# Kernel optimization log

Hardware: AMD Instinct MI355X
Metric: run time of the kernel (lower is better)

The kernel has to match this reference:

```python
import jax, jax.numpy as jnp
import numpy as np

RES = 32  # voxel grid resolution per axis (cfg.MODEL.NEURAL_POINTS.VOXEL_RES)


def upsample_ac(x, s):
    """Bilinear upsample with align_corners=True. x: [B,C,h,w] -> [B,C,h*s,w*s]."""
    if s == 1:
        return x
    B, C, h, w = x.shape
    H, W = h * s, w * s
    ys = jnp.arange(H, dtype=x.dtype) * ((h - 1) / (H - 1))
    xs = jnp.arange(W, dtype=x.dtype) * ((w - 1) / (W - 1))
    y0 = jnp.floor(ys).astype(jnp.int32)
    x0 = jnp.floor(xs).astype(jnp.int32)
    y1 = jnp.minimum(y0 + 1, h - 1)
    x1 = jnp.minimum(x0 + 1, w - 1)
    wy = (ys - y0.astype(x.dtype))[:, None]  # [H,1]
    wx = (xs - x0.astype(x.dtype))[None, :]  # [1,W]
    top = x[:, :, y0, :]
    bot = x[:, :, y1, :]
    a = top[..., x0]; b = top[..., x1]; c = bot[..., x0]; d = bot[..., x1]
    return (a * (1 - wx) + b * wx) * (1 - wy) + (c * (1 - wx) + d * wx) * wy


def vox_closest(pos):
    """construct_vox_points_closest: per occupied voxel, index of point closest to
    the voxel's point centroid. pos: [N,3] -> [RES^3] int32 indices."""
    N = pos.shape[0]
    Vn = RES ** 3
    mn = pos.min(0)
    mx = pos.max(0)
    vsz = (mx - mn) / RES  # obtain_voxel_size_based_grid_res
    coord = jnp.clip(jnp.floor((pos - mn) / vsz).astype(jnp.int32), 0, RES - 1)
    vid = (coord[:, 0] * RES + coord[:, 1]) * RES + coord[:, 2]  # [N]
    cnt = jax.ops.segment_sum(jnp.ones((N,), pos.dtype), vid, Vn)
    cen = jax.ops.segment_sum(pos, vid, Vn) / jnp.maximum(cnt, 1.0)[:, None]
    d = jnp.sum((pos - cen[vid]) ** 2, axis=-1)  # [N] dist^2 to own-voxel centroid
    dmin = jax.ops.segment_min(d, vid, Vn)
    cand = jnp.where(d <= dmin[vid], jnp.arange(N, dtype=jnp.int32), N)
    midx = jax.ops.segment_min(cand, vid, Vn)
    return jnp.where(midx >= N, 0, midx)  # guard (rare) empty voxels


def reference(rgb, f1, f2, f3, points_pos, points_dir, W1, b1, W2, b2, points_mask):
    V, _, H, W = rgb.shape
    N = V * H * W
    C = 59
    # valid_index = where(points_mask == 1) (mask is all ones -> identity gather)
    valid = jnp.nonzero(points_mask[0] == 1, size=N, fill_value=0)[0]
    pos = points_pos[0, valid]          # [N,3]
    pdir = points_dir[0, valid]         # [N,3]
    # project_point_feats: upsample each pyramid level to full res, concat channels
    ups = [upsample_ac(rgb, 1), upsample_ac(f1, 2), upsample_ac(f2, 4), upsample_ac(f3, 8)]
    pif = jnp.concatenate(ups, axis=1)                       # [V,59,H,W]
    pif = jnp.transpose(pif, (0, 2, 3, 1)).reshape(N, C)     # [N,59]
    color = jax.lax.stop_gradient(jnp.transpose(rgb, (0, 2, 3, 1)).reshape(N, 3))
    pif = pif[valid]
    color = color[valid]
    emb = jnp.concatenate([pif, pdir], axis=-1)              # [N,62]
    midx = vox_closest(pos)                                  # [32768]
    sel_emb = emb[midx]
    sel_pos = pos[midx]
    sel_color = color[midx]
    sel_dir = pdir[midx]
    # point_mlp (premlp_init): 62 -> 256 -> 256
    h = jax.nn.relu(sel_emb @ W1 + b1)
    points_embedding = h @ W2 + b2
    return points_embedding, sel_pos, sel_color, sel_dir


def setup_inputs() -> dict:
    key = jax.random.key(0)
    ks = jax.random.split(key, 10)
    V, H, W = 8, 240, 320
    N = V * H * W
    return {
        "rgb": jax.random.uniform(ks[0], (V, 3, H, W), jnp.float32),
        "f1": jax.random.normal(ks[1], (V, 8, H // 2, W // 2), jnp.float32),
        "f2": jax.random.normal(ks[2], (V, 16, H // 4, W // 4), jnp.float32),
        "f3": jax.random.normal(ks[3], (V, 32, H // 8, W // 8), jnp.float32),
        "points_pos": jax.random.uniform(ks[4], (1, N, 3), jnp.float32),
        "points_dir": jax.random.normal(ks[5], (1, N, 3), jnp.float32),
        "W1": jax.random.normal(ks[6], (62, 256), jnp.float32) * 0.05,
        "b1": jnp.zeros((256,), jnp.float32),
        "W2": jax.random.normal(ks[7], (256, 256), jnp.float32) * 0.05,
        "b2": jnp.zeros((256,), jnp.float32),
        "points_mask": jnp.ones((1, N), jnp.int32),
    }
```

## Files before the change

kernel.cpp:

```cpp
#include <hip/hip_runtime.h>
#include <hip/hip_bf16.h>
#include <limits.h>
#include <stddef.h>

#define NPTS   614400
#define RESV   32
#define NVOX   (RESV*RESV*RESV)
#define IMG_H  240
#define IMG_W  320
#define IMG_HW (IMG_H*IMG_W)
#define INF    __builtin_inff()
#define CAP    64
#define CAPP   32
#define SPILLCAP 4096

typedef __attribute__((ext_vector_type(8))) short short8;
typedef __attribute__((ext_vector_type(4))) short s16x4;
typedef __attribute__((ext_vector_type(4))) float f32x4;
typedef float f32x4u __attribute__((ext_vector_type(4), aligned(4)));

__device__ __forceinline__ float fadd_(float a, float b){
#pragma clang fp contract(off)
  return a + b;
}
__device__ __forceinline__ float fsub_(float a, float b){
#pragma clang fp contract(off)
  return a - b;
}
__device__ __forceinline__ float fmul_(float a, float b){
#pragma clang fp contract(off)
  return a * b;
}
__device__ __forceinline__ float fdiv_(float a, float b){
#pragma clang fp contract(off)
  return a / b;
}

__device__ __forceinline__ short f2bf(float x){
  __hip_bfloat16 h = __float2bfloat16(x);
  return *reinterpret_cast<short*>(&h);
}

__global__ void k_prep(int* __restrict__ cnt, int* __restrict__ spillcnt,
                       const float* __restrict__ W1, const float* __restrict__ W2,
                       short* __restrict__ W1t, short* __restrict__ W2t,
                       const float* __restrict__ pos,
                       f32x4* __restrict__ pmin, f32x4* __restrict__ pmax,
                       const float* __restrict__ f1, const float* __restrict__ f2,
                       const float* __restrict__ f3,
                       float* __restrict__ f1t, float* __restrict__ f2t,
                       float* __restrict__ f3t, int tposed){
  int gid = blockIdx.x*blockDim.x + threadIdx.x;
  int stride = gridDim.x*blockDim.x;
  if (gid < NVOX) cnt[gid] = 0;
  if (gid == 0) *spillcnt = 0;
  if (gid < 256*64){
    int n = gid >> 6, k = gid & 63;
    W1t[gid] = (k < 62) ? f2bf(W1[k*256 + n]) : (short)0;
  } else if (gid < 256*64 + 256*256){
    int j = gid - 256*64;
    int n = j >> 8, k = j & 255;
    W2t[j] = f2bf(W2[k*256 + n]);
  }

  if (tposed){
    for (int p = gid; p < 8*19200; p += stride){
      int img = p / 19200, pix = p - img*19200;
      const float* s = f1 + (size_t)img*8*19200 + pix;
      float r[8];
      #pragma unroll
      for (int c = 0; c < 8; c++) r[c] = s[(size_t)c*19200];
      float* d = f1t + (size_t)p*8;
      *(f32x4*)&d[0] = (f32x4){r[0],r[1],r[2],r[3]};
      *(f32x4*)&d[4] = (f32x4){r[4],r[5],r[6],r[7]};
    }
    for (int p = gid; p < 8*4800; p += stride){
      int img = p / 4800, pix = p - img*4800;
      const float* s = f2 + (size_t)img*16*4800 + pix;
      float* d = f2t + (size_t)p*16;
      #pragma unroll
      for (int cq = 0; cq < 4; cq++){
        f32x4 v = { s[(size_t)(4*cq+0)*4800], s[(size_t)(4*cq+1)*4800],
                    s[(size_t)(4*cq+2)*4800], s[(size_t)(4*cq+3)*4800] };
        *(f32x4*)&d[4*cq] = v;
      }
    }
    for (int p = gid; p < 8*1200; p += stride){
      int img = p / 1200, pix = p - img*1200;
      const float* s = f3 + (size_t)img*32*1200 + pix;
      float* d = f3t + (size_t)p*32;
      #pragma unroll
      for (int cq = 0; cq < 8; cq++){
        f32x4 v = { s[(size_t)(4*cq+0)*1200], s[(size_t)(4*cq+1)*1200],
                    s[(size_t)(4*cq+2)*1200], s[(size_t)(4*cq+3)*1200] };
        *(f32x4*)&d[4*cq] = v;
      }
    }
  }

  const f32x4* p4 = (const f32x4*)pos;
  float mn[3] = {  INF,  INF,  INF };
  float mx[3] = { -INF, -INF, -INF };
  for (int t = gid; t < NPTS/4; t += stride){
    f32x4 a = p4[3*t+0], b = p4[3*t+1], c = p4[3*t+2];
    mn[0] = fminf(mn[0], fminf(fminf(a.x, a.w), fminf(b.z, c.y)));
    mx[0] = fmaxf(mx[0], fmaxf(fmaxf(a.x, a.w), fmaxf(b.z, c.y)));
    mn[1] = fminf(mn[1], fminf(fminf(a.y, b.x), fminf(b.w, c.z)));
    mx[1] = fmaxf(mx[1], fmaxf(fmaxf(a.y, b.x), fmaxf(b.w, c.z)));
    mn[2] = fminf(mn[2], fminf(fminf(a.z, b.y), fminf(c.x, c.w)));
    mx[2] = fmaxf(mx[2], fmaxf(fmaxf(a.z, b.y), fmaxf(c.x, c.w)));
  }
  #pragma unroll
  for (int off = 32; off >= 1; off >>= 1){
    #pragma unroll
    for (int c = 0; c < 3; c++){
      mn[c] = fminf(mn[c], __shfl_down(mn[c], off, 64));
      mx[c] = fmaxf(mx[c], __shfl_down(mx[c], off, 64));
    }
  }
  __shared__ float smn[4][3], smx[4][3];
  int lane = threadIdx.x & 63, w = threadIdx.x >> 6;
  if (lane == 0){
    #pragma unroll
    for (int c = 0; c < 3; c++){ smn[w][c] = mn[c]; smx[w][c] = mx[c]; }
  }
  __syncthreads();
  if (threadIdx.x == 0){
    f32x4 a, b;
    a.x = fminf(fminf(smn[0][0], smn[1][0]), fminf(smn[2][0], smn[3][0]));
    a.y = fminf(fminf(smn[0][1], smn[1][1]), fminf(smn[2][1], smn[3][1]));
    a.z = fminf(fminf(smn[0][2], smn[1][2]), fminf(smn[2][2], smn[3][2]));
    a.w = 0.f;
    b.x = fmaxf(fmaxf(smx[0][0], smx[1][0]), fmaxf(smx[2][0], smx[3][0]));
    b.y = fmaxf(fmaxf(smx[0][1], smx[1][1]), fmaxf(smx[2][1], smx[3][1]));
    b.z = fmaxf(fmaxf(smx[0][2], smx[1][2]), fmaxf(smx[2][2], smx[3][2]));
    b.w = 0.f;
    pmin[blockIdx.x] = a;
    pmax[blockIdx.x] = b;
  }
}

__device__ __forceinline__ void reduce_minmax(const f32x4* __restrict__ pmin,
                                              const f32x4* __restrict__ pmax,
                                              float mn[3], float vsz[3]){
  int t = threadIdx.x;
  f32x4 a = pmin[t], b = pmin[t+256];
  f32x4 c = pmax[t], d = pmax[t+256];
  float lmn[3] = { fminf(a.x,b.x), fminf(a.y,b.y), fminf(a.z,b.z) };
  float lmx[3] = { fmaxf(c.x,d.x), fmaxf(c.y,d.y), fmaxf(c.z,d.z) };
  #pragma unroll
  for (int off = 32; off >= 1; off >>= 1){
    #pragma unroll
    for (int k = 0; k < 3; k++){
      lmn[k] = fminf(lmn[k], __shfl_xor(lmn[k], off, 64));
      lmx[k] = fmaxf(lmx[k], __shfl_xor(lmx[k], off, 64));
    }
  }
  __shared__ float smn[4][3], smx[4][3];
  int lane = t & 63, w = t >> 6;
  if (lane == 0){
    #pragma unroll
    for (int k = 0; k < 3; k++){ smn[w][k] = lmn[k]; smx[w][k] = lmx[k]; }
  }
  __syncthreads();
  #pragma unroll
  for (int k = 0; k < 3; k++){
    mn[k] = fminf(fminf(smn[0][k], smn[1][k]), fminf(smn[2][k], smn[3][k]));
    float mx = fmaxf(fmaxf(smx[0][k], smx[1][k]), fmaxf(smx[2][k], smx[3][k]));
    vsz[k] = fdiv_(fsub_(mx, mn[k]), 32.0f);
  }
}

__global__ void k_scatter(const float* __restrict__ pos,
                          const f32x4* __restrict__ pmin, const f32x4* __restrict__ pmax,
                          int* __restrict__ cnt, int* __restrict__ slots,
                          int* __restrict__ spillcnt, int2* __restrict__ spill,
                          f32x4* __restrict__ slotpos, int haspp){
  float mn[3], vsz[3];
  reduce_minmax(pmin, pmax, mn, vsz);

  int i = blockIdx.x*blockDim.x + threadIdx.x;
  float P[3] = { pos[3*i+0], pos[3*i+1], pos[3*i+2] };
  int v = 0;
  #pragma unroll
  for (int k = 0; k < 3; k++){
    float tt = fdiv_(fsub_(P[k], mn[k]), vsz[k]);
    int cc = (int)floorf(tt);
    cc = min(max(cc, 0), RESV-1);
    v = v*RESV + cc;
  }
  int p = atomicAdd(&cnt[v], 1);
  if (haspp){
    if (p < CAPP){
      f32x4 e = { P[0], P[1], P[2], __int_as_float(i) };
      slotpos[(size_t)v*CAPP + p] = e;
    } else if (p < CAP){
      slots[v*CAP + p] = i;
    } else {
      int sp = atomicAdd(spillcnt, 1);
      if (sp < SPILLCAP){ int2 e; e.x = v; e.y = i; spill[sp] = e; }
    }
  } else {
    if (p < CAP){
      slots[v*CAP + p] = i;
    } else {
      int sp = atomicAdd(spillcnt, 1);
      if (sp < SPILLCAP){ int2 e; e.x = v; e.y = i; spill[sp] = e; }
    }
  }
}

__launch_bounds__(256)
__global__ void k_voxfull(const int* __restrict__ cnt, const int* __restrict__ slots,
                          const int* __restrict__ spillcnt, const int2* __restrict__ spill,
                          const f32x4* __restrict__ slotpos, int haspp,
                          const float* __restrict__ pos,
                          const float* __restrict__ pdir, const float* __restrict__ rgb,
                          const float* __restrict__ f1, const float* __restrict__ f2,
                          const float* __restrict__ f3,
                          const float* __restrict__ f1t, const float* __restrict__ f2t,
                          const float* __restrict__ f3t, int tposed,
                          float* __restrict__ selpos, float* __restrict__ selcol,
                          float* __restrict__ seldir, short* __restrict__ emb){
  __shared__ __align__(16) int skey[4][64];
  __shared__ f32x4 sposl[4][64];
  int lane = threadIdx.x & 63;
  int wv   = threadIdx.x >> 6;
  int v = blockIdx.x*4 + wv;

  f32x4 q = {0.f, 0.f, 0.f, 0.f};
  if (haspp) q = slotpos[(size_t)v*CAPP + (lane & (CAPP-1))];
  int n = cnt[v];

  int m = 0;
  unsigned long long ball = 0;
  float px = 0.f, py = 0.f, pz = 0.f;

  if (n > CAP){
    if (lane == 0){
      int sc = min(*spillcnt, SPILLCAP);
      float sx = 0.f, sy = 0.f, sz = 0.f; int last = -1;
      for (int i = 0; i < n; i++){
        int best = INT_MAX;
        for (int j = 0; j < CAP; j++){
          int id = (haspp && j < CAPP) ? __float_as_int(slotpos[(size_t)v*CAPP + j].w)
                                       : slots[v*CAP + j];
          if (id > last && id < best) best = id;
        }
        for (int j = 0; j < sc; j++){
          int2 e = spill[j];
          if (e.x == v && e.y > last && e.y < best) best = e.y;
        }
        sx = fadd_(sx, pos[3*best+0]);
        sy = fadd_(sy, pos[3*best+1]);
        sz = fadd_(sz, pos[3*best+2]);
        last = best;
      }
      float cf = (float)n;
      float cx = fdiv_(sx, cf), cy = fdiv_(sy, cf), cz = fdiv_(sz, cf);
      float dmin = INF; int mm = 0;
      for (int j = 0; j < CAP + sc; j++){
        int id; int ok = 1;
        if (j < CAP){
          id = (haspp && j < CAPP) ? __float_as_int(slotpos[(size_t)v*CAPP + j].w)
                                   : slots[v*CAP + j];
        } else { int2 e = spill[j-CAP]; ok = (e.x == v); id = e.y; }
        if (!ok) continue;
        float dx = fsub_(pos[3*id+0], cx);
        float dy = fsub_(pos[3*id+1], cy);
        float dz = fsub_(pos[3*id+2], cz);
        float d  = fadd_(fadd_(fmul_(dx,dx), fmul_(dy,dy)), fmul_(dz,dz));
        if (d < dmin || (d == dmin && id < mm)){ dmin = d; mm = id; }
      }
      m = mm;
    }
    m = __shfl(m, 0, 64);
  } else {
    int key = INT_MAX;
    if (haspp && n <= CAPP){
      if (lane < n){
        px = q.x; py = q.y; pz = q.z;
        key = __float_as_int(q.w);
      }
    } else if (haspp){
      if (lane < CAPP){
        px = q.x; py = q.y; pz = q.z;
        key = __float_as_int(q.w);
      } else if (lane < n){
        key = slots[v*CAP + lane];
        if (key < NPTS-1){
          f32x4u qq = *(const f32x4u*)&pos[3*key];
          px = qq.x; py = qq.y; pz = qq.z;
        } else {
          px = pos[3*key+0]; py = pos[3*key+1]; pz = pos[3*key+2];
        }
      }
    } else {
      if (lane < n){
        key = slots[v*CAP + lane];
        if (key < NPTS-1){
          f32x4u qq = *(const f32x4u*)&pos[3*key];
          px = qq.x; py = qq.y; pz = qq.z;
        } else {
          px = pos[3*key+0]; py = pos[3*key+1]; pz = pos[3*key+2];
        }
      }
    }

    skey[wv][lane] = key;
    __builtin_amdgcn_wave_barrier();
    int r = 0;
    {
      int nq = (n + 3) >> 2;
      const int4* k4 = (const int4*)&skey[wv][0];
      for (int j = 0; j < nq; j++){
        int4 kk = k4[j];
        r += (kk.x < key) + (kk.y < key) + (kk.z < key) + (kk.w < key);
      }
    }
    if (lane < n){
      f32x4 e = { px, py, pz, 0.f };
      sposl[wv][r] = e;
    }
    __builtin_amdgcn_wave_barrier();

    float sx = 0.f, sy = 0.f, sz = 0.f;
    for (int i = 0; i < n; i++){
      f32x4 pp = sposl[wv][i];
      sx = fadd_(sx, pp.x);
      sy = fadd_(sy, pp.y);
      sz = fadd_(sz, pp.z);
    }
    float cf = fmaxf((float)n, 1.0f);
    float cx = fdiv_(sx, cf), cy = fdiv_(sy, cf), cz = fdiv_(sz, cf);

    float bd = INF; int bi = 0;
    if (lane < n){
      float dx = fsub_(px, cx), dy = fsub_(py, cy), dz = fsub_(pz, cz);
      bd = fadd_(fadd_(fmul_(dx,dx), fmul_(dy,dy)), fmul_(dz,dz));
      bi = key;
    }
    #pragma unroll
    for (int off = 32; off >= 1; off >>= 1){
      float od = __shfl_xor(bd, off, 64);
      int   oi = __shfl_xor(bi, off, 64);
      if (od < bd || (od == bd && oi < bi)){ bd = od; bi = oi; }
    }
    m = bi;
    ball = __ballot(lane < n && key == m);
  }

  float wx_ = 0.f, wy_ = 0.f, wz_ = 0.f;
  if (ball){
    int wl = (int)(__ffsll((long long)ball) - 1);
    wx_ = __shfl(px, wl, 64);
    wy_ = __shfl(py, wl, 64);
    wz_ = __shfl(pz, wl, 64);
  }

  int img = m / IMG_HW;
  int rem = m - img*IMG_HW;
  int y = rem / IMG_W;
  int x = rem - y*IMG_W;
  int ch = lane;
  float val;
  if (ch < 3){
    val = rgb[((img*3 + ch)*IMG_H + y)*IMG_W + x];
    selcol[3*v+ch] = val;
    float sp = ball ? ((ch == 0) ? wx_ : (ch == 1) ? wy_ : wz_) : pos[3*m+ch];
    selpos[3*v+ch] = sp;
  } else if (ch < 59){
    int lvl = (ch >= 27) ? 2 : ((ch >= 11) ? 1 : 0);
    int c   = ch - ((lvl == 0) ? 3 : ((lvl == 1) ? 11 : 27));
    int C   = 8 << lvl;
    int h   = 120 >> lvl, w = 160 >> lvl;
    float ry = (lvl == 0) ? (119.0f/239.0f) : ((lvl == 1) ? (59.0f/239.0f) : (29.0f/239.0f));
    float rx = (lvl == 0) ? (159.0f/319.0f) : ((lvl == 1) ? (79.0f/319.0f) : (39.0f/319.0f));
    float ys = (float)y * ry;
    float xs = (float)x * rx;
    int y0 = (int)floorf(ys);
    int x0 = (int)floorf(xs);
    int y1 = min(y0+1, h-1);
    int x1 = min(x0+1, w-1);
    float wy = ys - (float)y0;
    float wx = xs - (float)x0;
    float aa, bb, cc, dd;
    if (tposed){
      const float* ft = (lvl == 0) ? f1t : ((lvl == 1) ? f2t : f3t);
      const float* base = ft + (size_t)(img*h*w)*C + c;
      aa = base[(y0*w + x0)*C];
      bb = base[(y0*w + x1)*C];
      cc = base[(y1*w + x0)*C];
      dd = base[(y1*w + x1)*C];
    } else {
      const float* f = (lvl == 0) ? f1 : ((lvl == 1) ? f2 : f3);
      const float* plane = f + ((size_t)img*C + c)*(size_t)(h*w);
      aa = plane[y0*w + x0];
      bb = plane[y0*w + x1];
      cc = plane[y1*w + x0];
      dd = plane[y1*w + x1];
    }
    val = (aa*(1.f-wx) + bb*wx)*(1.f-wy) + (cc*(1.f-wx) + dd*wx)*wy;
  } else if (ch < 62){
    val = pdir[3*m + (ch-59)];
    seldir[3*v+(ch-59)] = val;
  } else {
    val = 0.f;
  }
  emb[(size_t)v*64 + ch] = f2bf(val);
}

#define MLP_BLOCKS 512
#define MLP_TILES  (NVOX/16/MLP_BLOCKS)
__launch_bounds__(256, 2)
__global__ void k_mlp(const short* __restrict__ emb, const short* __restrict__ W1t,
                      const float* __restrict__ b1f, const short* __restrict__ W2t,
                      const float* __restrict__ b2f, float* __restrict__ out){
  __shared__ short Hs[16][264];
  int t    = threadIdx.x;
  int lane = t & 63;
  int wv   = t >> 6;
  int m    = lane & 15;
  int q    = lane >> 4;

  short8 w1f[4][2], w2f[4][8];
  float  b1r[4][4], b2r[4];
  #pragma unroll
  for (int nt = 0; nt < 4; nt++){
    int n = wv*64 + nt*16 + m;
    #pragma unroll
    for (int kq = 0; kq < 2; kq++)
      w1f[nt][kq] = *(const short8*)&W1t[(size_t)n*64 + kq*32 + q*8];
    #pragma unroll
    for (int kq = 0; kq < 8; kq++)
      w2f[nt][kq] = *(const short8*)&W2t[(size_t)n*256 + kq*32 + q*8];
    #pragma unroll
    for (int i = 0; i < 4; i++)
      b1r[nt][i] = b1f[wv*64 + nt*16 + q*4 + i];
    b2r[nt] = b2f[n];
  }

  for (int tt = 0; tt < MLP_TILES; tt++){
    int row0 = (blockIdx.x*MLP_TILES + tt)*16;

    short8 ef0 = *(const short8*)&emb[(size_t)(row0 + m)*64 + q*8];
    short8 ef1 = *(const short8*)&emb[(size_t)(row0 + m)*64 + 32 + q*8];

    #pragma unroll
    for (int nt = 0; nt < 4; nt++){
      f32x4 c = {0.f, 0.f, 0.f, 0.f};
      c = __builtin_amdgcn_mfma_f32_16x16x32_bf16(w1f[nt][0], ef0, c, 0, 0, 0);
      c = __builtin_amdgcn_mfma_f32_16x16x32_bf16(w1f[nt][1], ef1, c, 0, 0, 0);
      s16x4 hv;
      #pragma unroll
      for (int i = 0; i < 4; i++)
        hv[i] = f2bf(fmaxf(c[i] + b1r[nt][i], 0.f));
      *(s16x4*)&Hs[m][wv*64 + nt*16 + q*4] = hv;
    }
    __syncthreads();

    f32x4 acc[4] = {{0,0,0,0},{0,0,0,0},{0,0,0,0},{0,0,0,0}};
    #pragma unroll
    for (int kq = 0; kq < 8; kq++){
      short8 af = *(const short8*)&Hs[m][kq*32 + q*8];
      #pragma unroll
      for (int nt = 0; nt < 4; nt++)
        acc[nt] = __builtin_amdgcn_mfma_f32_16x16x32_bf16(af, w2f[nt][kq], acc[nt], 0, 0, 0);
    }
    __syncthreads();

    #pragma unroll
    for (int nt = 0; nt < 4; nt++){
      int n = wv*64 + nt*16 + m;
      #pragma unroll
      for (int i = 0; i < 4; i++)
        out[(size_t)(row0 + q*4 + i)*256 + n] = acc[nt][i] + b2r[nt];
    }
  }
}

extern "C" void kernel_launch(void* const* d_in, const int* in_sizes, int n_in,
                              void* d_out, int out_size, void* d_ws, size_t ws_size,
                              hipStream_t stream){
  const float* rgb  = (const float*)d_in[0];
  const float* f1   = (const float*)d_in[1];
  const float* f2   = (const float*)d_in[2];
  const float* f3   = (const float*)d_in[3];
  const float* pos  = (const float*)d_in[4];
  const float* pdir = (const float*)d_in[5];
  const float* W1   = (const float*)d_in[6];
  const float* b1   = (const float*)d_in[7];
  const float* W2   = (const float*)d_in[8];
  const float* b2   = (const float*)d_in[9];

  float* out      = (float*)d_out;
  float* out_emb  = out;
  float* out_pos  = out + (size_t)NVOX*256;
  float* out_col  = out_pos + (size_t)NVOX*3;
  float* out_dir  = out_col + (size_t)NVOX*3;

  char* w = (char*)d_ws;
  int*   spillcnt = (int*)w;       w += 64;
  f32x4* pmin     = (f32x4*)w;     w += (size_t)512*16;
  f32x4* pmax     = (f32x4*)w;     w += (size_t)512*16;
  int*   cnt      = (int*)w;       w += (size_t)NVOX*4;
  short* W1t      = (short*)w;     w += (size_t)256*64*2;
  short* W2t      = (short*)w;     w += (size_t)256*256*2;
  short* emb      = (short*)w;     w += (size_t)NVOX*64*2;
  int2*  spill    = (int2*)w;      w += (size_t)SPILLCAP*8;
  int*   slots    = (int*)w;       w += (size_t)NVOX*CAP*4;
  float* f1t      = (float*)w;     w += (size_t)8*19200*8*4;
  float* f2t      = (float*)w;     w += (size_t)8*4800*16*4;
  float* f3t      = (float*)w;     w += (size_t)8*1200*32*4;
  int tposed = ((size_t)(w - (char*)d_ws) <= ws_size) ? 1 : 0;
  f32x4* slotpos  = (f32x4*)w;     w += (size_t)NVOX*CAPP*16;
  int haspp = ((size_t)(w - (char*)d_ws) <= ws_size) ? 1 : 0;

  k_prep    <<<512,    256, 0, stream>>>(cnt, spillcnt, W1, W2, W1t, W2t, pos, pmin, pmax,
                                         f1, f2, f3, f1t, f2t, f3t, tposed);
  k_scatter <<<NPTS/256, 256, 0, stream>>>(pos, pmin, pmax, cnt, slots, spillcnt, spill,
                                           slotpos, haspp);
  k_voxfull <<<NVOX/4, 256, 0, stream>>>(cnt, slots, spillcnt, spill, slotpos, haspp,
                                         pos, pdir, rgb, f1, f2, f3,
                                         f1t, f2t, f3t, tposed,
                                         out_pos, out_col, out_dir, emb);
  k_mlp     <<<MLP_BLOCKS, 256, 0, stream>>>(emb, W1t, b1, W2t, b2, out_emb);
}
```

Before: 195.7 us.

## Replace global-atomic point scatter with two-pass bucketed binning via shared-memory counters

Points are first binned into 128 coarse buckets (256 voxels each) using per-block shared histograms and one global atomic per bucket per block. A second kernel, with one block per bucket, recomputes each point's voxel and takes slot indices from shared-memory counters before writing per-voxel counts out. This removes the contended global atomicAdd on per-voxel counters and spreads writes more locally. It adds an extra kernel and a bucket buffer placed in the output embedding region, relying on that region being overwritten later. It also adds an overflow path that every block must scan.

New measurement: 172.9 us (median of 2 runs). 11.6% less time.

```diff
diff --git a/kernel.cpp b/kernel.cpp
--- a/kernel.cpp
+++ b/kernel.cpp
@@ -13,6 +13,9 @@
 #define CAP    64
 #define CAPP   32
 #define SPILLCAP 4096
+#define NBKT   128
+#define BCAP   6144
+#define BOVFCAP 4096
 
 typedef __attribute__((ext_vector_type(8))) short short8;
 typedef __attribute__((ext_vector_type(4))) short s16x4;
@@ -42,6 +45,7 @@
 }
 
 __global__ void k_prep(int* __restrict__ cnt, int* __restrict__ spillcnt,
+                       int* __restrict__ gbase,
                        const float* __restrict__ W1, const float* __restrict__ W2,
                        short* __restrict__ W1t, short* __restrict__ W2t,
                        const float* __restrict__ pos,
@@ -53,7 +57,8 @@
   int gid = blockIdx.x*blockDim.x + threadIdx.x;
   int stride = gridDim.x*blockDim.x;
   if (gid < NVOX) cnt[gid] = 0;
-  if (gid == 0) *spillcnt = 0;
+  if (gid == 0){ spillcnt[0] = 0; spillcnt[1] = 0; }
+  if (gid < NBKT) gbase[gid] = 0;
   if (gid < 256*64){
     int n = gid >> 6, k = gid & 63;
     W1t[gid] = (k < 62) ? f2bf(W1[k*256 + n]) : (short)0;
@@ -171,43 +176,149 @@
   }
 }
 
-__global__ void k_scatter(const float* __restrict__ pos,
-                          const f32x4* __restrict__ pmin, const f32x4* __restrict__ pmax,
-                          int* __restrict__ cnt, int* __restrict__ slots,
-                          int* __restrict__ spillcnt, int2* __restrict__ spill,
-                          f32x4* __restrict__ slotpos, int haspp){
+__global__ void k_bucket(const float* __restrict__ pos,
+                         const f32x4* __restrict__ pmin, const f32x4* __restrict__ pmax,
+                         int* __restrict__ gbase, f32x4* __restrict__ bucketbuf,
+                         int* __restrict__ bovfcnt, f32x4* __restrict__ bovf){
   float mn[3], vsz[3];
   reduce_minmax(pmin, pmax, mn, vsz);
 
-  int i = blockIdx.x*blockDim.x + threadIdx.x;
-  float P[3] = { pos[3*i+0], pos[3*i+1], pos[3*i+2] };
-  int v = 0;
+  __shared__ int h[NBKT], cur[NBKT];
+  int t = threadIdx.x;
+  if (t < NBKT) h[t] = 0;
+  __syncthreads();
+
+  int base = blockIdx.x*blockDim.x + t;
+  const f32x4* p4 = (const f32x4*)pos;
+  f32x4 a = p4[3*base+0], b = p4[3*base+1], c = p4[3*base+2];
+  float X[4] = {a.x, a.w, b.z, c.y};
+  float Y[4] = {a.y, b.x, b.w, c.z};
+  float Z[4] = {a.z, b.y, c.x, c.w};
+  int vox[4];
+  #pragma unroll
+  for (int j = 0; j < 4; j++){
+    float P[3] = {X[j], Y[j], Z[j]};
+    int v = 0;
+    #pragma unroll
+    for (int k = 0; k < 3; k++){
+      float tt = fdiv_(fsub_(P[k], mn[k]), vsz[k]);
+      int cc = (int)floorf(tt);
+      cc = min(max(cc, 0), RESV-1);
+      v = v*RESV + cc;
+    }
+    vox[j] = v;
+    atomicAdd(&h[v >> 8], 1);
+  }
+  __syncthreads();
+  if (t < NBKT) cur[t] = atomicAdd(&gbase[t], h[t]);
+  __syncthreads();
+  #pragma unroll
+  for (int j = 0; j < 4; j++){
+    int i = 4*base + j;
+    int bk = vox[j] >> 8;
+    int r = atomicAdd(&cur[bk], 1);
+    f32x4 e = { X[j], Y[j], Z[j], __int_as_float(i) };
+    if (r < BCAP){
+      bucketbuf[(size_t)bk*BCAP + r] = e;
+    } else {
+      int so = atomicAdd(bovfcnt, 1);
+      if (so < BOVFCAP) bovf[so] = e;
+    }
+  }
+}
+
+__launch_bounds__(512)
+__global__ void k_vox2(const f32x4* __restrict__ pmin, const f32x4* __restrict__ pmax,
+                       const int* __restrict__ gbase, const f32x4* __restrict__ bucketbuf,
+                       const int* __restrict__ bovfcnt, const f32x4* __restrict__ bovf,
+                       int* __restrict__ cnt, int* __restrict__ slots,
+                       int* __restrict__ spillcnt, int2* __restrict__ spill,
+                       f32x4* __restrict__ slotpos, int haspp){
+  __shared__ float smn[8][3], smx[8][3];
+  __shared__ int cnt_s[256];
+  int t = threadIdx.x;
+  if (t < 256) cnt_s[t] = 0;
+
+  {
+    int tt = t & 255;
+    f32x4 a = pmin[tt], b = pmin[tt+256];
+    f32x4 c = pmax[tt], d = pmax[tt+256];
+    float lmn[3] = { fminf(a.x,b.x), fminf(a.y,b.y), fminf(a.z,b.z) };
+    float lmx[3] = { fmaxf(c.x,d.x), fmaxf(c.y,d.y), fmaxf(c.z,d.z) };
+    #pragma unroll
+    for (int off = 32; off >= 1; off >>= 1){
+      #pragma unroll
+      for (int k = 0; k < 3; k++){
+        lmn[k] = fminf(lmn[k], __shfl_xor(lmn[k], off, 64));
+        lmx[k] = fmaxf(lmx[k], __shfl_xor(lmx[k], off, 64));
+      }
+    }
+    int lane = t & 63, w = t >> 6;
+    if (lane == 0){
+      #pragma unroll
+      for (int k = 0; k < 3; k++){ smn[w][k] = lmn[k]; smx[w][k] = lmx[k]; }
+    }
+  }
+  __syncthreads();
+  float mn[3], vsz[3];
   #pragma unroll
   for (int k = 0; k < 3; k++){
-    float tt = fdiv_(fsub_(P[k], mn[k]), vsz[k]);
-    int cc = (int)floorf(tt);
-    cc = min(max(cc, 0), RESV-1);
-    v = v*RESV + cc;
-  }
-  int p = atomicAdd(&cnt[v], 1);
-  if (haspp){
-    if (p < CAPP){
-      f32x4 e = { P[0], P[1], P[2], __int_as_float(i) };
-      slotpos[(size_t)v*CAPP + p] = e;
+    float lo = smn[0][k], hi = smx[0][k];
+    #pragma unroll
+    for (int w = 1; w < 8; w++){ lo = fminf(lo, smn[w][k]); hi = fmaxf(hi, smx[w][k]); }
+    mn[k] = lo;
+    vsz[k] = fdiv_(fsub_(hi, lo), 32.0f);
+  }
+
+  int b = blockIdx.x;
+  int nb = min(gbase[b], BCAP);
+  for (int j = t; j < nb; j += 512){
+    f32x4 rec = bucketbuf[(size_t)b*BCAP + j];
+    float P[3] = {rec.x, rec.y, rec.z};
+    int v = 0;
+    #pragma unroll
+    for (int k = 0; k < 3; k++){
+      float tt = fdiv_(fsub_(P[k], mn[k]), vsz[k]);
+      int cc = (int)floorf(tt);
+      cc = min(max(cc, 0), RESV-1);
+      v = v*RESV + cc;
+    }
+    int p = atomicAdd(&cnt_s[v & 255], 1);
+    if (haspp && p < CAPP){
+      slotpos[(size_t)v*CAPP + p] = rec;
     } else if (p < CAP){
-      slots[v*CAP + p] = i;
+      slots[v*CAP + p] = __float_as_int(rec.w);
     } else {
       int sp = atomicAdd(spillcnt, 1);
-      if (sp < SPILLCAP){ int2 e; e.x = v; e.y = i; spill[sp] = e; }
-    }
-  } else {
-    if (p < CAP){
-      slots[v*CAP + p] = i;
-    } else {
-      int sp = atomicAdd(spillcnt, 1);
-      if (sp < SPILLCAP){ int2 e; e.x = v; e.y = i; spill[sp] = e; }
-    }
-  }
+      if (sp < SPILLCAP){ int2 e; e.x = v; e.y = __float_as_int(rec.w); spill[sp] = e; }
+    }
+  }
+  int bc = min(*bovfcnt, BOVFCAP);
+  for (int j = t; j < bc; j += 512){
+    f32x4 rec = bovf[j];
+    float P[3] = {rec.x, rec.y, rec.z};
+    int v = 0;
+    #pragma unroll
+    for (int k = 0; k < 3; k++){
+      float tt = fdiv_(fsub_(P[k], mn[k]), vsz[k]);
+      int cc = (int)floorf(tt);
+      cc = min(max(cc, 0), RESV-1);
+      v = v*RESV + cc;
+    }
+    if ((v >> 8) == b){
+      int p = atomicAdd(&cnt_s[v & 255], 1);
+      if (haspp && p < CAPP){
+        slotpos[(size_t)v*CAPP + p] = rec;
+      } else if (p < CAP){
+        slots[v*CAP + p] = __float_as_int(rec.w);
+      } else {
+        int sp = atomicAdd(spillcnt, 1);
+        if (sp < SPILLCAP){ int2 e; e.x = v; e.y = __float_as_int(rec.w); spill[sp] = e; }
+      }
+    }
+  }
+  __syncthreads();
+  if (t < 256) cnt[(b << 8) + t] = cnt_s[t];
 }
 
 __launch_bounds__(256)
@@ -499,6 +610,11 @@
   float* out_col  = out_pos + (size_t)NVOX*3;
   float* out_dir  = out_col + (size_t)NVOX*3;
 
+  char* ob = (char*)out_emb;
+  f32x4* bucketbuf = (f32x4*)ob;
+  f32x4* bovf      = (f32x4*)(ob + (size_t)NBKT*BCAP*16);
+  int*   gbase     = (int*)  (ob + (size_t)NBKT*BCAP*16 + (size_t)BOVFCAP*16);
+
   char* w = (char*)d_ws;
   int*   spillcnt = (int*)w;       w += 64;
   f32x4* pmin     = (f32x4*)w;     w += (size_t)512*16;
@@ -516,13 +632,18 @@
   f32x4* slotpos  = (f32x4*)w;     w += (size_t)NVOX*CAPP*16;
   int haspp = ((size_t)(w - (char*)d_ws) <= ws_size) ? 1 : 0;
 
-  k_prep    <<<512,    256, 0, stream>>>(cnt, spillcnt, W1, W2, W1t, W2t, pos, pmin, pmax,
-                                         f1, f2, f3, f1t, f2t, f3t, tposed);
-  k_scatter <<<NPTS/256, 256, 0, stream>>>(pos, pmin, pmax, cnt, slots, spillcnt, spill,
-                                           slotpos, haspp);
-  k_voxfull <<<NVOX/4, 256, 0, stream>>>(cnt, slots, spillcnt, spill, slotpos, haspp,
-                                         pos, pdir, rgb, f1, f2, f3,
-                                         f1t, f2t, f3t, tposed,
-                                         out_pos, out_col, out_dir, emb);
-  k_mlp     <<<MLP_BLOCKS, 256, 0, stream>>>(emb, W1t, b1, W2t, b2, out_emb);
-}
+  int* bovfcnt = spillcnt + 1;
+
+  k_prep   <<<512,       256, 0, stream>>>(cnt, spillcnt, gbase, W1, W2, W1t, W2t,
+                                           pos, pmin, pmax,
+                                           f1, f2, f3, f1t, f2t, f3t, tposed);
+  k_bucket <<<NPTS/1024, 256, 0, stream>>>(pos, pmin, pmax, gbase, bucketbuf,
+                                           bovfcnt, bovf);
+  k_vox2   <<<NBKT,      512, 0, stream>>>(pmin, pmax, gbase, bucketbuf, bovfcnt, bovf,
+                                           cnt, slots, spillcnt, spill, slotpos, haspp);
+  k_voxfull<<<NVOX/4,    256, 0, stream>>>(cnt, slots, spillcnt, spill, slotpos, haspp,
+                                           pos, pdir, rgb, f1, f2, f3,
+                                           f1t, f2t, f3t, tposed,
+                                           out_pos, out_col, out_dir, emb);
+  k_mlp    <<<MLP_BLOCKS,256, 0, stream>>>(emb, W1t, b1, W2t, b2, out_emb);
+}
```
